# Optimization experiments

Hardware: AMD Instinct MI355X
Metric: run time of the kernel (lower is better)

The kernel has to match this reference:

```python
import jax, jax.numpy as jnp
import numpy as np

EMBED_DIM = 1024
SEQ_LEN = 2048
BATCH = 4


def setup_inputs() -> dict:
    key = jax.random.key(0)
    kx, kq, kk, kv = jax.random.split(key, 4)
    scale = 1.0 / np.sqrt(EMBED_DIM)
    x = jax.random.normal(kx, (BATCH, SEQ_LEN, EMBED_DIM), dtype=jnp.float32)
    # nn.Linear weights are [out, in]; stored transposed-application here
    W_query = jax.random.normal(kq, (EMBED_DIM, EMBED_DIM), dtype=jnp.float32) * scale
    W_key = jax.random.normal(kk, (EMBED_DIM, EMBED_DIM), dtype=jnp.float32) * scale
    W_value = jax.random.normal(kv, (EMBED_DIM, EMBED_DIM), dtype=jnp.float32) * scale
    return {"x": x, "W_query": W_query, "W_key": W_key, "W_value": W_value}


def reference(x, W_query, W_key, W_value):
    # x: [B, S, D]; W_*: [D_out, D_in] (torch nn.Linear layout -> y = x @ W.T)
    B, S, D = x.shape
    q = jnp.einsum("bsd,ed->bse", x, W_query)
    k = jnp.einsum("bsd,ed->bse", x, W_key)
    v = jnp.einsum("bsd,ed->bse", x, W_value)
    scores = jnp.einsum("bqd,bkd->bqk", q, k)  # [B, S, S]
    causal = jnp.triu(jnp.ones((S, S), dtype=bool), k=1)  # True above diagonal
    scores = jnp.where(causal, -jnp.inf, scores)
    weights = jax.nn.softmax(scores / jnp.sqrt(jnp.asarray(D, x.dtype)), axis=-1)
    return jnp.einsum("bqk,bkd->bqd", weights, v)
```

## Files before the change

kernel.cpp:

```cpp
#include <hip/hip_runtime.h>
#include <stdint.h>

typedef __bf16 bf16_t;
typedef __bf16 bf16x4 __attribute__((ext_vector_type(4)));
typedef __bf16 bf16x8 __attribute__((ext_vector_type(8)));
typedef float  f32x4  __attribute__((ext_vector_type(4)));

#define AS1 __attribute__((address_space(1)))
#define AS3 __attribute__((address_space(3)))

__device__ __forceinline__ void gld_lds16(const bf16_t* g, void* s) {
  __builtin_amdgcn_global_load_lds((const AS1 uint32_t*)g, (AS3 uint32_t*)s, 16, 0, 0);
}

__global__ __launch_bounds__(256) void convert_all_kernel(
    const float* __restrict__ X,  const float* __restrict__ Wq,
    const float* __restrict__ Wk, const float* __restrict__ Wv,
    bf16_t* __restrict__ Xc, bf16_t* __restrict__ Wqc,
    bf16_t* __restrict__ Wkc, bf16_t* __restrict__ Wvc) {
  const int blk = blockIdx.x;
  const float* src; bf16_t* dst; int base;
  if (blk < 4096)      { src = X;  dst = Xc;  base = 0;    }
  else if (blk < 4608) { src = Wq; dst = Wqc; base = 4096; }
  else if (blk < 5120) { src = Wk; dst = Wkc; base = 4608; }
  else                 { src = Wv; dst = Wvc; base = 5120; }
  const int i = ((blk - base) * 256 + threadIdx.x) * 8;
  const float4 a = ((const float4*)(src + i))[0];
  const float4 b = ((const float4*)(src + i))[1];
  bf16x8 v;
  v[0] = (bf16_t)a.x; v[1] = (bf16_t)a.y; v[2] = (bf16_t)a.z; v[3] = (bf16_t)a.w;
  v[4] = (bf16_t)b.x; v[5] = (bf16_t)b.y; v[6] = (bf16_t)b.z; v[7] = (bf16_t)b.w;
  *(bf16x8*)(dst + i) = v;
}

__device__ __forceinline__ void gemm_thin_core(
    const bf16_t* __restrict__ A, int lda,
    const bf16_t* __restrict__ B, int ldb,
    int m0, int n0, int kEnd,
    char* lds, f32x4 acc[4][4])
{
  const int tid  = threadIdx.x;
  const int lane = tid & 63;
  const int wave = tid >> 6;
  const int wm = (wave >> 2) * 64;
  const int wn = (wave & 3) * 64;
  const int fr = lane & 15;
  const int ck = lane >> 4;

  const int srow = tid >> 2;
  const int sch  = tid & 3;
  const int kg   = (sch ^ ((srow >> 1) & 3)) * 8;
  const int dstA = srow * 64 + sch * 16;
  const int dstB = dstA;

  const bf16_t* Ar  = A + (size_t)(m0 + srow) * lda + kg;
  const bf16_t* Br0 = B + (size_t)(n0 + srow) * ldb + kg;
  const bf16_t* Br1 = B + (size_t)(n0 + srow + 128) * ldb + kg;

  int aoff[4], boff[4];
#pragma unroll
  for (int i = 0; i < 4; ++i) {
    const int ra = wm + i * 16 + fr;
    const int rb = wn + i * 16 + fr;
    aoff[i] = ra * 64 + ((ck ^ ((ra >> 1) & 3)) * 16);
    boff[i] = rb * 64 + ((ck ^ ((rb >> 1) & 3)) * 16);
  }

  gld_lds16(Ar, lds + dstA);
  gld_lds16(Br0, lds + 16384 + dstB);
  gld_lds16(Br1, lds + 16384 + 8192 + dstB);

  const int NK = kEnd >> 5;
  int cur = 0;
  for (int t = 0; t < NK; ++t) {
    const int nxt = cur ^ 1;
    if (t + 1 < NK) {
      const int ko = (t + 1) * 32;
      gld_lds16(Ar + ko, lds + nxt * 8192 + dstA);
      gld_lds16(Br0 + ko, lds + 16384 + nxt * 16384 + dstB);
      gld_lds16(Br1 + ko, lds + 16384 + nxt * 16384 + 8192 + dstB);
      asm volatile("s_waitcnt vmcnt(3)" ::: "memory");
    } else {
      asm volatile("s_waitcnt vmcnt(0)" ::: "memory");
    }
    __builtin_amdgcn_sched_barrier(0);
    __builtin_amdgcn_s_barrier();
    __builtin_amdgcn_sched_barrier(0);

    const char* Ab = lds + cur * 8192;
    const char* Bb = lds + 16384 + cur * 16384;
    bf16x8 af[4], bfv[4];
#pragma unroll
    for (int i = 0; i < 4; ++i) {
      af[i]  = *(const bf16x8*)(Ab + aoff[i]);
      bfv[i] = *(const bf16x8*)(Bb + boff[i]);
    }
    asm volatile("s_waitcnt lgkmcnt(0)" ::: "memory");
    __builtin_amdgcn_sched_barrier(0);
    __builtin_amdgcn_s_setprio(1);
#pragma unroll
    for (int mi = 0; mi < 4; ++mi)
#pragma unroll
      for (int ni = 0; ni < 4; ++ni)
        acc[mi][ni] = __builtin_amdgcn_mfma_f32_16x16x32_bf16(
            af[mi], bfv[ni], acc[mi][ni], 0, 0, 0);
    __builtin_amdgcn_s_setprio(0);
    __builtin_amdgcn_sched_barrier(0);
    __builtin_amdgcn_s_barrier();
    __builtin_amdgcn_sched_barrier(0);
    cur = nxt;
  }
}

__device__ __forceinline__ void gemm_bt_core(
    const bf16_t* __restrict__ A, int lda,
    const bf16_t* __restrict__ B, int ldb,
    int m0, int n0, int kBeg, int kEnd,
    bf16_t* As, bf16_t* Bs, f32x4 acc[4][4])
{
  const int lane = threadIdx.x & 63;
  const int wave = threadIdx.x >> 6;
  const int wm = (wave >> 1) * 64;
  const int wn = (wave & 1) * 64;
  const int fr = lane & 15;
  const int ck = lane >> 4;

  const int off0 = wave * 2048 + lane * 16;
  const int row0 = wave * 32 + (lane >> 2);
  const int row1 = row0 + 16;
  const int kg   = ((lane & 3) ^ ((row0 >> 1) & 3)) * 8;

  const bf16_t* Ar0 = A + (size_t)(m0 + row0) * lda + kg;
  const bf16_t* Ar1 = A + (size_t)(m0 + row1) * lda + kg;
  const bf16_t* Br0 = B + (size_t)(n0 + row0) * ldb + kg;
  const bf16_t* Br1 = B + (size_t)(n0 + row1) * ldb + kg;

  int aoff[4], boff[4];
#pragma unroll
  for (int i = 0; i < 4; ++i) {
    const int ra = wm + i * 16 + fr;
    const int rb = wn + i * 16 + fr;
    aoff[i] = ra * 64 + ((ck ^ ((ra >> 1) & 3)) * 16);
    boff[i] = rb * 64 + ((ck ^ ((rb >> 1) & 3)) * 16);
  }

  gld_lds16(Ar0 + kBeg, (char*)As + off0);
  gld_lds16(Ar1 + kBeg, (char*)As + off0 + 1024);
  gld_lds16(Br0 + kBeg, (char*)Bs + off0);
  gld_lds16(Br1 + kBeg, (char*)Bs + off0 + 1024);

  int cur = 0;
  for (int kt = kBeg; kt < kEnd; kt += 32) {
    const int nxt = cur ^ 1;
    if (kt + 32 < kEnd) {
      gld_lds16(Ar0 + kt + 32, (char*)As + nxt * 8192 + off0);
      gld_lds16(Ar1 + kt + 32, (char*)As + nxt * 8192 + off0 + 1024);
      gld_lds16(Br0 + kt + 32, (char*)Bs + nxt * 8192 + off0);
      gld_lds16(Br1 + kt + 32, (char*)Bs + nxt * 8192 + off0 + 1024);
      asm volatile("s_waitcnt vmcnt(4)" ::: "memory");
    } else {
      asm volatile("s_waitcnt vmcnt(0)" ::: "memory");
    }
    __builtin_amdgcn_sched_barrier(0);
    __builtin_amdgcn_s_barrier();
    __builtin_amdgcn_sched_barrier(0);

    bf16x8 af[4], bfv[4];
#pragma unroll
    for (int mi = 0; mi < 4; ++mi)
      af[mi] = *(const bf16x8*)((char*)As + cur * 8192 + aoff[mi]);
#pragma unroll
    for (int ni = 0; ni < 4; ++ni)
      bfv[ni] = *(const bf16x8*)((char*)Bs + cur * 8192 + boff[ni]);
    __builtin_amdgcn_s_setprio(1);
#pragma unroll
    for (int mi = 0; mi < 4; ++mi)
#pragma unroll
      for (int ni = 0; ni < 4; ++ni)
        acc[mi][ni] = __builtin_amdgcn_mfma_f32_16x16x32_bf16(
            af[mi], bfv[ni], acc[mi][ni], 0, 0, 0);
    __builtin_amdgcn_s_setprio(0);

    asm volatile("s_waitcnt lgkmcnt(0)" ::: "memory");
    __builtin_amdgcn_sched_barrier(0);
    __builtin_amdgcn_s_barrier();
    __builtin_amdgcn_sched_barrier(0);
    cur = nxt;
  }
}

__global__ __launch_bounds__(512) void qkv_kernel(
    const bf16_t* __restrict__ X,
    const bf16_t* __restrict__ Wq, const bf16_t* __restrict__ Wk,
    const bf16_t* __restrict__ Wv,
    bf16_t* __restrict__ Q, bf16_t* __restrict__ K, bf16_t* __restrict__ Vt)
{
  __shared__ bf16_t smem[24576];
  const int bid = blockIdx.x;
  const int z   = bid >> 8;
  const int t   = bid & 255;
  const int m0  = (t >> 2) * 128;
  const int n0  = (t & 3) * 256;
  const bf16_t* W = (z == 0) ? Wq : (z == 1) ? Wk : Wv;

  f32x4 acc[4][4] = {};
  gemm_thin_core(X, 1024, W, 1024, m0, n0, 1024, (char*)smem, acc);

  const int tid  = threadIdx.x;
  const int lane = tid & 63;
  const int wave = tid >> 6;
  const int wm = (wave >> 2) * 64, wn = (wave & 3) * 64;

  if (z < 2) {
    bf16_t* Out = z ? K : Q;
#pragma unroll
    for (int mi = 0; mi < 4; ++mi)
#pragma unroll
      for (int r = 0; r < 4; ++r) {
        const int row = m0 + wm + mi * 16 + (lane >> 4) * 4 + r;
#pragma unroll
        for (int ni = 0; ni < 4; ++ni) {
          const int col = n0 + wn + ni * 16 + (lane & 15);
          Out[(size_t)row * 1024 + col] = (bf16_t)acc[mi][ni][r];
        }
      }
  } else {
    const int b  = m0 >> 11;
    const int s0 = m0 & 2047;
    bf16_t* Vtb = Vt + (size_t)b * 1024 * 2048;
    bf16_t (*tb)[136] = (bf16_t(*)[136])smem;
#pragma unroll
    for (int h = 0; h < 4; ++h) {
      __syncthreads();
      if ((wave & 3) == h) {
#pragma unroll
        for (int mi = 0; mi < 4; ++mi)
#pragma unroll
          for (int ni = 0; ni < 4; ++ni) {
            const int c    = ni * 16 + (lane & 15);
            const int rowl = wm + mi * 16 + (lane >> 4) * 4;
            bf16x4 v;
            v[0] = (bf16_t)acc[mi][ni][0]; v[1] = (bf16_t)acc[mi][ni][1];
            v[2] = (bf16_t)acc[mi][ni][2]; v[3] = (bf16_t)acc[mi][ni][3];
            *(bf16x4*)&tb[c][rowl] = v;
          }
      }
      __syncthreads();
#pragma unroll
      for (int i = 0; i < 2; ++i) {
        const int idx = tid + 512 * i;
        const int d   = idx >> 4;
        const int ch  = idx & 15;
        bf16x8 vv = *(const bf16x8*)&tb[d][ch * 8];
        *(bf16x8*)(Vtb + (size_t)(n0 + h * 64 + d) * 2048 + s0 + ch * 8) = vv;
      }
    }
  }
}

__global__ __launch_bounds__(512) void scores_exp_kernel(
    const bf16_t* __restrict__ Q, const bf16_t* __restrict__ K,
    bf16_t* __restrict__ P, float* __restrict__ partials)
{
  const int L = blockIdx.x;
  const int c   = L & 7;
  const int idx = L >> 3;
  const int batch = idx / 9;
  const int r     = idx % 9;
  const int lo    = (c >> 1) + 1;
  int mt, nt;
  if (r < lo) { mt = c;      nt = r; }
  else        { mt = 15 - c; nt = r - lo; }
  const int m0 = mt * 128;
  const int n0 = nt * 256;
  __shared__ bf16_t smem[24576];
  const bf16_t* Qb = Q + (size_t)batch * 2048 * 1024;
  const bf16_t* Kb = K + (size_t)batch * 2048 * 1024;
  bf16_t* Pb = P + (size_t)batch * 2048 * 2048;
  float* lp  = partials + (size_t)batch * 16 * 2048;

  f32x4 acc[4][4] = {};
  gemm_thin_core(Qb, 1024, Kb, 1024, m0, n0, 1024, (char*)smem, acc);

  const int tid  = threadIdx.x;
  const int lane = tid & 63;
  const int wave = tid >> 6;
  const int wm = (wave >> 2) * 64, wn = (wave & 3) * 64;
  float (*rs4)[128] = (float(*)[128])smem;
  const float cst = 0.04508422f;
#pragma unroll
  for (int mi = 0; mi < 4; ++mi)
#pragma unroll
    for (int rr = 0; rr < 4; ++rr) {
      const int lrow = wm + mi * 16 + (lane >> 4) * 4 + rr;
      const int row  = m0 + lrow;
      float rs = 0.f;
#pragma unroll
      for (int ni = 0; ni < 4; ++ni) {
        const int col = n0 + wn + ni * 16 + (lane & 15);
        float p = exp2f(acc[mi][ni][rr] * cst);
        if (col > row) p = 0.f;
        const bf16_t pb = (bf16_t)p;
        Pb[(size_t)row * 2048 + col] = pb;
        rs += (float)pb;
      }
      rs += __shfl_xor(rs, 1);
      rs += __shfl_xor(rs, 2);
      rs += __shfl_xor(rs, 4);
      rs += __shfl_xor(rs, 8);
      if ((lane & 15) == 0) rs4[wave & 3][lrow] = rs;
    }
  __syncthreads();
  if (tid < 256) {
    const int row = tid & 127;
    const int s   = tid >> 7;
    lp[(size_t)(2 * nt + s) * 2048 + m0 + row] =
        rs4[2 * s][row] + rs4[2 * s + 1][row];
  }
}

__global__ __launch_bounds__(256) void lsum_kernel(
    const float* __restrict__ partials, float* __restrict__ Linv)
{
  const int id  = blockIdx.x * 256 + threadIdx.x;
  const int z   = id >> 11;
  const int row = id & 2047;
  const float* lp = partials + (size_t)z * 16 * 2048;
  const int tmax = row >> 7;
  float l = 0.f;
  for (int kt = 0; kt <= tmax; ++kt) l += lp[kt * 2048 + row];
  Linv[id] = 1.f / l;
}

__global__ __launch_bounds__(256) void pv_kernel(
    const bf16_t* __restrict__ P, const bf16_t* __restrict__ Vt,
    const float* __restrict__ Linv, float* __restrict__ out)
{
  __shared__ bf16_t smem[4 * 128 * 32];
  bf16_t* As = smem;
  bf16_t* Bs = smem + 2 * 128 * 32;
  const int L  = blockIdx.x;
  const int c  = L & 7;
  const int s  = (L >> 3) & 31;
  const int hi = L >> 8;
  const int zb = s & 3;
  const int dt = s >> 2;
  const int mt = hi ? (15 - c) : c;
  const int m0 = mt * 128;
  const int n0 = dt * 128;
  const bf16_t* Pb  = P  + (size_t)zb * 2048 * 2048;
  const bf16_t* Vtb = Vt + (size_t)zb * 1024 * 2048;
  const float* li = Linv + (size_t)zb * 2048;
  float* ob = out + (size_t)zb * 2048 * 1024;

  f32x4 acc[4][4] = {};
  gemm_bt_core(Pb, 2048, Vtb, 2048, m0, n0, 0, m0 + 128, As, Bs, acc);

  const int lane = threadIdx.x & 63;
  const int wave = threadIdx.x >> 6;
  const int wm = (wave >> 1) * 64, wn = (wave & 1) * 64;
#pragma unroll
  for (int mi = 0; mi < 4; ++mi)
#pragma unroll
    for (int r = 0; r < 4; ++r) {
      const int row = m0 + wm + mi * 16 + (lane >> 4) * 4 + r;
      const float inv = li[row];
#pragma unroll
      for (int ni = 0; ni < 4; ++ni) {
        const int col = n0 + wn + ni * 16 + (lane & 15);
        ob[(size_t)row * 1024 + col] = acc[mi][ni][r] * inv;
      }
    }
}

extern "C" void kernel_launch(void* const* d_in, const int* in_sizes, int n_in,
                              void* d_out, int out_size, void* d_ws, size_t ws_size,
                              hipStream_t stream) {
  const float* X  = (const float*)d_in[0];
  const float* Wq = (const float*)d_in[1];
  const float* Wk = (const float*)d_in[2];
  const float* Wv = (const float*)d_in[3];
  float* out = (float*)d_out;
  char* ws = (char*)d_ws;

  const size_t MB = 1024 * 1024;
  bf16_t* Q    = (bf16_t*)(ws + 0 * MB);
  bf16_t* K    = (bf16_t*)(ws + 16 * MB);
  bf16_t* Vt   = (bf16_t*)(ws + 32 * MB);
  bf16_t* Xc   = (bf16_t*)(ws + 48 * MB);
  bf16_t* Wqc  = (bf16_t*)(ws + 64 * MB);
  bf16_t* Wkc  = (bf16_t*)(ws + 66 * MB);
  bf16_t* Wvc  = (bf16_t*)(ws + 68 * MB);
  bf16_t* P    = (bf16_t*)(ws + 48 * MB);
  float*  Lp   = (float*)(ws + 80 * MB);
  float*  Linv = (float*)(ws + 80 * MB + 512 * 1024);

  convert_all_kernel<<<dim3(5632), 256, 0, stream>>>(X, Wq, Wk, Wv, Xc, Wqc, Wkc, Wvc);
  qkv_kernel<<<dim3(768), 512, 0, stream>>>(Xc, Wqc, Wkc, Wvc, Q, K, Vt);
  scores_exp_kernel<<<dim3(288), 512, 0, stream>>>(Q, K, P, Lp);
  lsum_kernel<<<dim3(32), 256, 0, stream>>>(Lp, Linv);
  pv_kernel<<<dim3(512), 256, 0, stream>>>(P, Vt, Linv, out);
}
```

Baseline: 225.6 us.

## Split QKV projection into QK and V kernels; use 128x128 triangular scores tiles

After: 233.1 us. +3.3%, slower.

```diff
diff --git a/kernel.cpp b/kernel.cpp
--- a/kernel.cpp
+++ b/kernel.cpp
@@ -1,5 +1,6 @@
 #include <hip/hip_runtime.h>
 #include <stdint.h>
+#include <math.h>
 
 typedef __bf16 bf16_t;
 typedef __bf16 bf16x4 __attribute__((ext_vector_type(4)));
@@ -189,11 +190,10 @@
   }
 }
 
-__global__ __launch_bounds__(512) void qkv_kernel(
+__global__ __launch_bounds__(512) void qk_kernel(
     const bf16_t* __restrict__ X,
     const bf16_t* __restrict__ Wq, const bf16_t* __restrict__ Wk,
-    const bf16_t* __restrict__ Wv,
-    bf16_t* __restrict__ Q, bf16_t* __restrict__ K, bf16_t* __restrict__ Vt)
+    bf16_t* __restrict__ Q, bf16_t* __restrict__ K)
 {
   __shared__ bf16_t smem[24576];
   const int bid = blockIdx.x;
@@ -201,104 +201,116 @@
   const int t   = bid & 255;
   const int m0  = (t >> 2) * 128;
   const int n0  = (t & 3) * 256;
-  const bf16_t* W = (z == 0) ? Wq : (z == 1) ? Wk : Wv;
+  const bf16_t* W = z ? Wk : Wq;
 
   f32x4 acc[4][4] = {};
   gemm_thin_core(X, 1024, W, 1024, m0, n0, 1024, (char*)smem, acc);
+
+  const int lane = threadIdx.x & 63;
+  const int wave = threadIdx.x >> 6;
+  const int wm = (wave >> 2) * 64, wn = (wave & 3) * 64;
+  bf16_t* Out = z ? K : Q;
+#pragma unroll
+  for (int mi = 0; mi < 4; ++mi)
+#pragma unroll
+    for (int r = 0; r < 4; ++r) {
+      const int row = m0 + wm + mi * 16 + (lane >> 4) * 4 + r;
+#pragma unroll
+      for (int ni = 0; ni < 4; ++ni) {
+        const int col = n0 + wn + ni * 16 + (lane & 15);
+        Out[(size_t)row * 1024 + col] = (bf16_t)acc[mi][ni][r];
+      }
+    }
+}
+
+__global__ __launch_bounds__(512) void v_kernel(
+    const bf16_t* __restrict__ X, const bf16_t* __restrict__ Wv,
+    bf16_t* __restrict__ Vt)
+{
+  __shared__ bf16_t smem[24576];
+  const int t   = blockIdx.x;
+  const int m0  = (t >> 2) * 128;
+  const int n0  = (t & 3) * 256;
+
+  f32x4 acc[4][4] = {};
+  gemm_thin_core(X, 1024, Wv, 1024, m0, n0, 1024, (char*)smem, acc);
 
   const int tid  = threadIdx.x;
   const int lane = tid & 63;
   const int wave = tid >> 6;
-  const int wm = (wave >> 2) * 64, wn = (wave & 3) * 64;
-
-  if (z < 2) {
-    bf16_t* Out = z ? K : Q;
-#pragma unroll
-    for (int mi = 0; mi < 4; ++mi)
-#pragma unroll
-      for (int r = 0; r < 4; ++r) {
-        const int row = m0 + wm + mi * 16 + (lane >> 4) * 4 + r;
+  const int wm = (wave >> 2) * 64;
+
+  const int b  = m0 >> 11;
+  const int s0 = m0 & 2047;
+  bf16_t* Vtb = Vt + (size_t)b * 1024 * 2048;
+  bf16_t (*tb)[136] = (bf16_t(*)[136])smem;
+#pragma unroll
+  for (int h = 0; h < 4; ++h) {
+    __syncthreads();
+    if ((wave & 3) == h) {
+#pragma unroll
+      for (int mi = 0; mi < 4; ++mi)
 #pragma unroll
         for (int ni = 0; ni < 4; ++ni) {
-          const int col = n0 + wn + ni * 16 + (lane & 15);
-          Out[(size_t)row * 1024 + col] = (bf16_t)acc[mi][ni][r];
+          const int c    = ni * 16 + (lane & 15);
+          const int rowl = wm + mi * 16 + (lane >> 4) * 4;
+          bf16x4 v;
+          v[0] = (bf16_t)acc[mi][ni][0]; v[1] = (bf16_t)acc[mi][ni][1];
+          v[2] = (bf16_t)acc[mi][ni][2]; v[3] = (bf16_t)acc[mi][ni][3];
+          *(bf16x4*)&tb[c][rowl] = v;
         }
-      }
-  } else {
-    const int b  = m0 >> 11;
-    const int s0 = m0 & 2047;
-    bf16_t* Vtb = Vt + (size_t)b * 1024 * 2048;
-    bf16_t (*tb)[136] = (bf16_t(*)[136])smem;
-#pragma unroll
-    for (int h = 0; h < 4; ++h) {
-      __syncthreads();
-      if ((wave & 3) == h) {
-#pragma unroll
-        for (int mi = 0; mi < 4; ++mi)
-#pragma unroll
-          for (int ni = 0; ni < 4; ++ni) {
-            const int c    = ni * 16 + (lane & 15);
-            const int rowl = wm + mi * 16 + (lane >> 4) * 4;
-            bf16x4 v;
-            v[0] = (bf16_t)acc[mi][ni][0]; v[1] = (bf16_t)acc[mi][ni][1];
-            v[2] = (bf16_t)acc[mi][ni][2]; v[3] = (bf16_t)acc[mi][ni][3];
-            *(bf16x4*)&tb[c][rowl] = v;
-          }
-      }
-      __syncthreads();
-#pragma unroll
-      for (int i = 0; i < 2; ++i) {
-        const int idx = tid + 512 * i;
-        const int d   = idx >> 4;
-        const int ch  = idx & 15;
-        bf16x8 vv = *(const bf16x8*)&tb[d][ch * 8];
-        *(bf16x8*)(Vtb + (size_t)(n0 + h * 64 + d) * 2048 + s0 + ch * 8) = vv;
-      }
-    }
-  }
-}
-
-__global__ __launch_bounds__(512) void scores_exp_kernel(
+    }
+    __syncthreads();
+#pragma unroll
+    for (int i = 0; i < 2; ++i) {
+      const int idx = tid + 512 * i;
+      const int d   = idx >> 4;
+      const int ch  = idx & 15;
+      bf16x8 vv = *(const bf16x8*)&tb[d][ch * 8];
+      *(bf16x8*)(Vtb + (size_t)(n0 + h * 64 + d) * 2048 + s0 + ch * 8) = vv;
+    }
+  }
+}
+
+__global__ __launch_bounds__(256) void scores_exp_kernel(
     const bf16_t* __restrict__ Q, const bf16_t* __restrict__ K,
     bf16_t* __restrict__ P, float* __restrict__ partials)
 {
-  const int L = blockIdx.x;
-  const int c   = L & 7;
-  const int idx = L >> 3;
-  const int batch = idx / 9;
-  const int r     = idx % 9;
-  const int lo    = (c >> 1) + 1;
-  int mt, nt;
-  if (r < lo) { mt = c;      nt = r; }
-  else        { mt = 15 - c; nt = r - lo; }
+  const int t = blockIdx.x;
+  int mt = (int)((sqrtf(8.f * t + 1.f) - 1.f) * 0.5f);
+  while ((mt + 1) * (mt + 2) / 2 <= t) ++mt;
+  while (mt * (mt + 1) / 2 > t) --mt;
+  const int nt = t - mt * (mt + 1) / 2;
   const int m0 = mt * 128;
-  const int n0 = nt * 256;
-  __shared__ bf16_t smem[24576];
+  const int n0 = nt * 128;
+  __shared__ bf16_t smem[4 * 128 * 32];
+  __shared__ float rowsum[2][128];
+  bf16_t* As = smem;
+  bf16_t* Bs = smem + 2 * 128 * 32;
+  const int batch = blockIdx.y;
   const bf16_t* Qb = Q + (size_t)batch * 2048 * 1024;
   const bf16_t* Kb = K + (size_t)batch * 2048 * 1024;
   bf16_t* Pb = P + (size_t)batch * 2048 * 2048;
-  float* lp  = partials + (size_t)batch * 16 * 2048;
+  float* lp  = partials + ((size_t)batch * 16 + nt) * 2048;
 
   f32x4 acc[4][4] = {};
-  gemm_thin_core(Qb, 1024, Kb, 1024, m0, n0, 1024, (char*)smem, acc);
-
-  const int tid  = threadIdx.x;
-  const int lane = tid & 63;
-  const int wave = tid >> 6;
-  const int wm = (wave >> 2) * 64, wn = (wave & 3) * 64;
-  float (*rs4)[128] = (float(*)[128])smem;
+  gemm_bt_core(Qb, 1024, Kb, 1024, m0, n0, 0, 1024, As, Bs, acc);
+
+  const int lane = threadIdx.x & 63;
+  const int wave = threadIdx.x >> 6;
+  const int wm = (wave >> 1) * 64, wn = (wave & 1) * 64;
   const float cst = 0.04508422f;
 #pragma unroll
   for (int mi = 0; mi < 4; ++mi)
 #pragma unroll
-    for (int rr = 0; rr < 4; ++rr) {
-      const int lrow = wm + mi * 16 + (lane >> 4) * 4 + rr;
+    for (int r = 0; r < 4; ++r) {
+      const int lrow = wm + mi * 16 + (lane >> 4) * 4 + r;
       const int row  = m0 + lrow;
       float rs = 0.f;
 #pragma unroll
       for (int ni = 0; ni < 4; ++ni) {
         const int col = n0 + wn + ni * 16 + (lane & 15);
-        float p = exp2f(acc[mi][ni][rr] * cst);
+        float p = exp2f(acc[mi][ni][r] * cst);
         if (col > row) p = 0.f;
         const bf16_t pb = (bf16_t)p;
         Pb[(size_t)row * 2048 + col] = pb;
@@ -308,15 +320,11 @@
       rs += __shfl_xor(rs, 2);
       rs += __shfl_xor(rs, 4);
       rs += __shfl_xor(rs, 8);
-      if ((lane & 15) == 0) rs4[wave & 3][lrow] = rs;
+      if ((lane & 15) == 0) rowsum[wave & 1][lrow] = rs;
     }
   __syncthreads();
-  if (tid < 256) {
-    const int row = tid & 127;
-    const int s   = tid >> 7;
-    lp[(size_t)(2 * nt + s) * 2048 + m0 + row] =
-        rs4[2 * s][row] + rs4[2 * s + 1][row];
-  }
+  if (threadIdx.x < 128)
+    lp[m0 + threadIdx.x] = rowsum[0][threadIdx.x] + rowsum[1][threadIdx.x];
 }
 
 __global__ __launch_bounds__(256) void lsum_kernel(
@@ -328,7 +336,11 @@
   const float* lp = partials + (size_t)z * 16 * 2048;
   const int tmax = row >> 7;
   float l = 0.f;
-  for (int kt = 0; kt <= tmax; ++kt) l += lp[kt * 2048 + row];
+#pragma unroll
+  for (int kt = 0; kt < 16; ++kt) {
+    const float v = lp[kt * 2048 + row];
+    l += (kt <= tmax) ? v : 0.f;
+  }
   Linv[id] = 1.f / l;
 }
 
@@ -396,8 +408,9 @@
   float*  Linv = (float*)(ws + 80 * MB + 512 * 1024);
 
   convert_all_kernel<<<dim3(5632), 256, 0, stream>>>(X, Wq, Wk, Wv, Xc, Wqc, Wkc, Wvc);
-  qkv_kernel<<<dim3(768), 512, 0, stream>>>(Xc, Wqc, Wkc, Wvc, Q, K, Vt);
-  scores_exp_kernel<<<dim3(288), 512, 0, stream>>>(Q, K, P, Lp);
+  qk_kernel<<<dim3(512), 512, 0, stream>>>(Xc, Wqc, Wkc, Q, K);
+  v_kernel<<<dim3(256), 512, 0, stream>>>(Xc, Wvc, Vt);
+  scores_exp_kernel<<<dim3(136, 4), 256, 0, stream>>>(Q, K, P, Lp);
   lsum_kernel<<<dim3(32), 256, 0, stream>>>(Lp, Linv);
   pv_kernel<<<dim3(512), 256, 0, stream>>>(P, Vt, Linv, out);
 }
```
